# Optimization experiments

Measured on AMD Instinct MI355X. Metric: run time of the kernel, lower is better.

## Reference

```python
import jax, jax.numpy as jnp
import numpy as np

BATCH = 2048
NUM_FIELDS = 32
EMBED = 64
NPAIRS = NUM_FIELDS * (NUM_FIELDS - 1) // 2  # 496
# static pair indices (i < j), same order as the torch double loop
ROW, COL = np.triu_indices(NUM_FIELDS, k=1)
ROW = jnp.asarray(ROW)
COL = jnp.asarray(COL)


def setup_inputs() -> dict:
    key = jax.random.key(0)
    k1, k2 = jax.random.split(key)
    emb_inputs = jax.random.normal(k1, (BATCH, NUM_FIELDS, EMBED), dtype=jnp.float32)
    # xavier_normal_ on kernel of shape (E, NC2, E): fan_in = NC2*E (dims[1:]), fan_out = E*E... 
    # torch: fan_in = size(1)*receptive = NPAIRS*EMBED? torch uses size(1)*prod(size[2:]) = NPAIRS*EMBED,
    # fan_out = size(0)*prod(size[2:]) = EMBED*EMBED; std = sqrt(2/(fan_in+fan_out))
    fan_in = NPAIRS * EMBED
    fan_out = EMBED * EMBED
    std = float(np.sqrt(2.0 / (fan_in + fan_out)))
    kernel = jax.random.normal(k2, (EMBED, NPAIRS, EMBED), dtype=jnp.float32) * std
    return {"emb_inputs": emb_inputs, "kernel": kernel}


def reference(emb_inputs, kernel):
    # emb_inputs: (B, N, E); kernel: (E, NC2, E)
    p = emb_inputs[:, ROW]  # (B, NC2, E)
    q = emb_inputs[:, COL]  # (B, NC2, E)
    # torch: kp[b,i,pair] = sum_j p[b,pair,j] * kernel[i,pair,j]; out[b,pair] = sum_i kp*q
    kp = jnp.einsum('bpj,ipj->bpi', p, kernel)  # (B, NC2, E) -- avoids (B,E,NC2,E) blowup
    outputs = jnp.sum(kp * q, axis=-1)          # (B, NC2)
    return outputs[:, None, :]                  # (B, 1, NC2)
```

## Files before the change

### kernel.cpp

```cpp
#include <hip/hip_runtime.h>
#include <hip/hip_bf16.h>

#define BATCH   2048
#define NFIELDS 32
#define EMBED   64
#define NPAIRS  496

typedef __attribute__((ext_vector_type(8))) short bf16x8;
typedef __attribute__((ext_vector_type(4))) float f32x4;

__device__ __forceinline__ unsigned short f2bf(float x) {
    unsigned int u = __float_as_uint(x);
    unsigned int r = 0x7fffu + ((u >> 16) & 1u);
    return (unsigned short)((u + r) >> 16);
}
__device__ __forceinline__ bf16x8 cvt8(const float* p) {
    float4 v0 = *(const float4*)p;
    float4 v1 = *(const float4*)(p + 4);
    bf16x8 o;
    o[0]=(short)f2bf(v0.x); o[1]=(short)f2bf(v0.y); o[2]=(short)f2bf(v0.z); o[3]=(short)f2bf(v0.w);
    o[4]=(short)f2bf(v1.x); o[5]=(short)f2bf(v1.y); o[6]=(short)f2bf(v1.z); o[7]=(short)f2bf(v1.w);
    return o;
}

__global__ __launch_bounds__(256) void convert_prepass(
    const float* __restrict__ emb, const float* __restrict__ kern,
    unsigned short* __restrict__ embB, unsigned short* __restrict__ kernB)
{
    const int EMB4 = BATCH * NFIELDS * EMBED / 4;
    const int KER4 = EMBED * NPAIRS * EMBED / 4;
    int t = blockIdx.x * blockDim.x + threadIdx.x;
    if (t < EMB4) {
        float4 v = ((const float4*)emb)[t];
        ushort4 o;
        o.x = f2bf(v.x); o.y = f2bf(v.y); o.z = f2bf(v.z); o.w = f2bf(v.w);
        *(ushort4*)(embB + (size_t)t * 4) = o;
    } else if (t < EMB4 + KER4) {
        int u = t - EMB4;
        int j4   = u & 15;
        int rest = u >> 4;
        int p = rest % NPAIRS;
        int i = rest / NPAIRS;
        float4 v = *(const float4*)(kern + (size_t)i * (NPAIRS*EMBED) + (size_t)p * EMBED + j4*4);
        ushort4 o;
        o.x = f2bf(v.x); o.y = f2bf(v.y); o.z = f2bf(v.z); o.w = f2bf(v.w);
        *(ushort4*)(kernB + (size_t)p * 4096 + i * 64 + j4 * 4) = o;
    }
}

template<bool PRE>
__global__ __launch_bounds__(256) void opn_main(
    const void* __restrict__ embP, const void* __restrict__ kernP,
    const float* __restrict__ embF, float* __restrict__ out)
{
    const int chunk = blockIdx.x;
    const int bt    = blockIdx.y;
    const int tid   = threadIdx.x;
    const int wave  = tid >> 6, lane = tid & 63;
    const int col   = lane & 15, quad = lane >> 4;
    const int pair  = chunk * 4 + wave;

    int r = 0, s = 0;
    while (pair >= s + (NFIELDS - 1 - r)) { s += NFIELDS - 1 - r; ++r; }
    const int c = r + 1 + (pair - s);

    __shared__ __align__(16) float Otile[128][4];

    bf16x8 kfr[4][2];
    if (PRE) {
        const unsigned short* kb = (const unsigned short*)kernP + (size_t)pair * 4096;
        #pragma unroll
        for (int nt = 0; nt < 4; ++nt)
            #pragma unroll
            for (int ks = 0; ks < 2; ++ks)
                kfr[nt][ks] = *(const bf16x8*)(kb + (nt*16 + col) * 64 + ks*32 + quad*8);
    } else {
        const float* kf = (const float*)kernP;
        #pragma unroll
        for (int nt = 0; nt < 4; ++nt)
            #pragma unroll
            for (int ks = 0; ks < 2; ++ks)
                kfr[nt][ks] = cvt8(kf + (size_t)(nt*16 + col) * (NPAIRS*EMBED)
                                     + (size_t)pair * EMBED + ks*32 + quad*8);
    }

    #pragma unroll 2
    for (int it = 0; it < 8; ++it) {
        const int brow = bt * 128 + it * 16 + col;

        bf16x8 bfr0, bfr1;
        if (PRE) {
            const unsigned short* eb = (const unsigned short*)embP
                                     + ((size_t)brow * NFIELDS + r) * EMBED;
            bfr0 = *(const bf16x8*)(eb + quad*8);
            bfr1 = *(const bf16x8*)(eb + 32 + quad*8);
        } else {
            const float* ef = (const float*)embP + ((size_t)brow * NFIELDS + r) * EMBED;
            bfr0 = cvt8(ef + quad*8);
            bfr1 = cvt8(ef + 32 + quad*8);
        }

        const float* qp = embF + ((size_t)brow * NFIELDS + c) * EMBED + quad*4;
        f32x4 q0 = *(const f32x4*)(qp);
        f32x4 q1 = *(const f32x4*)(qp + 16);
        f32x4 q2 = *(const f32x4*)(qp + 32);
        f32x4 q3 = *(const f32x4*)(qp + 48);

        float partial = 0.f;
        #pragma unroll
        for (int nt = 0; nt < 4; ++nt) {
            f32x4 acc = {0.f, 0.f, 0.f, 0.f};
            acc = __builtin_amdgcn_mfma_f32_16x16x32_bf16(kfr[nt][0], bfr0, acc, 0, 0, 0);
            acc = __builtin_amdgcn_mfma_f32_16x16x32_bf16(kfr[nt][1], bfr1, acc, 0, 0, 0);
            f32x4 qq = (nt == 0) ? q0 : (nt == 1) ? q1 : (nt == 2) ? q2 : q3;
            partial += acc[0]*qq[0] + acc[1]*qq[1] + acc[2]*qq[2] + acc[3]*qq[3];
        }
        partial += __shfl_xor(partial, 16, 64);
        partial += __shfl_xor(partial, 32, 64);
        if (quad == 0) Otile[it*16 + col][wave] = partial;
    }
    __syncthreads();

    if (tid < 128) {
        f32x4 o = *(const f32x4*)&Otile[tid][0];
        *(f32x4*)&out[((size_t)(bt*128 + tid)) * NPAIRS + chunk*4] = o;
    }
}

extern "C" void kernel_launch(void* const* d_in, const int* in_sizes, int n_in,
                              void* d_out, int out_size, void* d_ws, size_t ws_size,
                              hipStream_t stream) {
    const float* emb  = (const float*)d_in[0];
    const float* kern = (const float*)d_in[1];
    float* out = (float*)d_out;

    const size_t embElems  = (size_t)BATCH * NFIELDS * EMBED;
    const size_t kernElems = (size_t)EMBED * NPAIRS * EMBED;
    const size_t need = (embElems + kernElems) * sizeof(unsigned short);

    dim3 grid(NPAIRS / 4, BATCH / 128);
    if (ws_size >= need) {
        unsigned short* embB  = (unsigned short*)d_ws;
        unsigned short* kernB = embB + embElems;
        int total4 = (int)((embElems + kernElems) / 4);
        convert_prepass<<<(total4 + 255) / 256, 256, 0, stream>>>(emb, kern, embB, kernB);
        opn_main<true><<<grid, 256, 0, stream>>>((const void*)embB, (const void*)kernB, emb, out);
    } else {
        opn_main<false><<<grid, 256, 0, stream>>>((const void*)emb, (const void*)kern, emb, out);
    }
}
```

Before: 125.8 us.

## Fuse bf16 conversion into main kernel, halve batch tile, swizzle block order

Drops the separate fp32-to-bf16 conversion prepass and workspace, so the main kernel reads fp32 embeddings and kernel weights directly and converts them in registers. The batch tile per block shrinks from 128 to 64 rows, doubling the grid to 3968 one-dimensional blocks, with a swizzled block index to group blocks for cache locality. This removes a launch and a full read/write pass over both tensors. In exchange, fp32 data is re-read at twice the width, and each block now reloads and converts its kernel fragments while amortising them over fewer rows.

```diff
diff --git a/kernel.cpp b/kernel.cpp
--- a/kernel.cpp
+++ b/kernel.cpp
@@ -23,84 +23,43 @@
     return o;
 }
 
-__global__ __launch_bounds__(256) void convert_prepass(
+__global__ __launch_bounds__(256) void opn_fused(
     const float* __restrict__ emb, const float* __restrict__ kern,
-    unsigned short* __restrict__ embB, unsigned short* __restrict__ kernB)
+    float* __restrict__ out)
 {
-    const int EMB4 = BATCH * NFIELDS * EMBED / 4;
-    const int KER4 = EMBED * NPAIRS * EMBED / 4;
-    int t = blockIdx.x * blockDim.x + threadIdx.x;
-    if (t < EMB4) {
-        float4 v = ((const float4*)emb)[t];
-        ushort4 o;
-        o.x = f2bf(v.x); o.y = f2bf(v.y); o.z = f2bf(v.z); o.w = f2bf(v.w);
-        *(ushort4*)(embB + (size_t)t * 4) = o;
-    } else if (t < EMB4 + KER4) {
-        int u = t - EMB4;
-        int j4   = u & 15;
-        int rest = u >> 4;
-        int p = rest % NPAIRS;
-        int i = rest / NPAIRS;
-        float4 v = *(const float4*)(kern + (size_t)i * (NPAIRS*EMBED) + (size_t)p * EMBED + j4*4);
-        ushort4 o;
-        o.x = f2bf(v.x); o.y = f2bf(v.y); o.z = f2bf(v.z); o.w = f2bf(v.w);
-        *(ushort4*)(kernB + (size_t)p * 4096 + i * 64 + j4 * 4) = o;
-    }
-}
+    const int bid = blockIdx.x;
+    const int swz = (bid & 7) * 496 + (bid >> 3);
+    const int chunk = swz >> 5;
+    const int bt    = swz & 31;
 
-template<bool PRE>
-__global__ __launch_bounds__(256) void opn_main(
-    const void* __restrict__ embP, const void* __restrict__ kernP,
-    const float* __restrict__ embF, float* __restrict__ out)
-{
-    const int chunk = blockIdx.x;
-    const int bt    = blockIdx.y;
-    const int tid   = threadIdx.x;
-    const int wave  = tid >> 6, lane = tid & 63;
-    const int col   = lane & 15, quad = lane >> 4;
-    const int pair  = chunk * 4 + wave;
+    const int tid  = threadIdx.x;
+    const int wave = tid >> 6, lane = tid & 63;
+    const int col  = lane & 15, quad = lane >> 4;
+    const int pair = chunk * 4 + wave;
 
     int r = 0, s = 0;
     while (pair >= s + (NFIELDS - 1 - r)) { s += NFIELDS - 1 - r; ++r; }
     const int c = r + 1 + (pair - s);
 
-    __shared__ __align__(16) float Otile[128][4];
+    __shared__ __align__(16) float Otile[64][4];
 
     bf16x8 kfr[4][2];
-    if (PRE) {
-        const unsigned short* kb = (const unsigned short*)kernP + (size_t)pair * 4096;
+    #pragma unroll
+    for (int nt = 0; nt < 4; ++nt)
         #pragma unroll
-        for (int nt = 0; nt < 4; ++nt)
-            #pragma unroll
-            for (int ks = 0; ks < 2; ++ks)
-                kfr[nt][ks] = *(const bf16x8*)(kb + (nt*16 + col) * 64 + ks*32 + quad*8);
-    } else {
-        const float* kf = (const float*)kernP;
-        #pragma unroll
-        for (int nt = 0; nt < 4; ++nt)
-            #pragma unroll
-            for (int ks = 0; ks < 2; ++ks)
-                kfr[nt][ks] = cvt8(kf + (size_t)(nt*16 + col) * (NPAIRS*EMBED)
-                                     + (size_t)pair * EMBED + ks*32 + quad*8);
-    }
+        for (int ks = 0; ks < 2; ++ks)
+            kfr[nt][ks] = cvt8(kern + (size_t)(nt*16 + col) * (NPAIRS*EMBED)
+                                 + (size_t)pair * EMBED + ks*32 + quad*8);
 
-    #pragma unroll 2
-    for (int it = 0; it < 8; ++it) {
-        const int brow = bt * 128 + it * 16 + col;
+    #pragma unroll
+    for (int it = 0; it < 4; ++it) {
+        const int brow = bt * 64 + it * 16 + col;
 
-        bf16x8 bfr0, bfr1;
-        if (PRE) {
-            const unsigned short* eb = (const unsigned short*)embP
-                                     + ((size_t)brow * NFIELDS + r) * EMBED;
-            bfr0 = *(const bf16x8*)(eb + quad*8);
-            bfr1 = *(const bf16x8*)(eb + 32 + quad*8);
-        } else {
-            const float* ef = (const float*)embP + ((size_t)brow * NFIELDS + r) * EMBED;
-            bfr0 = cvt8(ef + quad*8);
-            bfr1 = cvt8(ef + 32 + quad*8);
-        }
+        const float* ef = emb + ((size_t)brow * NFIELDS + r) * EMBED;
+        bf16x8 bfr0 = cvt8(ef + quad*8);
+        bf16x8 bfr1 = cvt8(ef + 32 + quad*8);
 
-        const float* qp = embF + ((size_t)brow * NFIELDS + c) * EMBED + quad*4;
+        const float* qp = emb + ((size_t)brow * NFIELDS + c) * EMBED + quad*4;
         f32x4 q0 = *(const f32x4*)(qp);
         f32x4 q1 = *(const f32x4*)(qp + 16);
         f32x4 q2 = *(const f32x4*)(qp + 32);
@@ -121,9 +80,9 @@
     }
     __syncthreads();
 
-    if (tid < 128) {
+    if (tid < 64) {
         f32x4 o = *(const f32x4*)&Otile[tid][0];
-        *(f32x4*)&out[((size_t)(bt*128 + tid)) * NPAIRS + chunk*4] = o;
+        *(f32x4*)&out[((size_t)(bt*64 + tid)) * NPAIRS + chunk*4] = o;
     }
 }
 
@@ -134,18 +93,5 @@
     const float* kern = (const float*)d_in[1];
     float* out = (float*)d_out;
 
-    const size_t embElems  = (size_t)BATCH * NFIELDS * EMBED;
-    const size_t kernElems = (size_t)EMBED * NPAIRS * EMBED;
-    const size_t need = (embElems + kernElems) * sizeof(unsigned short);
-
-    dim3 grid(NPAIRS / 4, BATCH / 128);
-    if (ws_size >= need) {
-        unsigned short* embB  = (unsigned short*)d_ws;
-        unsigned short* kernB = embB + embElems;
-        int total4 = (int)((embElems + kernElems) / 4);
-        convert_prepass<<<(total4 + 255) / 256, 256, 0, stream>>>(emb, kern, embB, kernB);
-        opn_main<true><<<grid, 256, 0, stream>>>((const void*)embB, (const void*)kernB, emb, out);
-    } else {
-        opn_main<false><<<grid, 256, 0, stream>>>((const void*)emb, (const void*)kern, emb, out);
-    }
+    opn_fused<<<dim3(3968), 256, 0, stream>>>(emb, kern, out);
 }
```

After: 151.6 us. 20.5% more time.

## Halve batch tile, swizzle block order for XCD locality, read q from bf16

Applied to the files above, without the earlier changes.

Each block now covers 64 batch rows instead of 128, on a flattened 3968-block grid. Block IDs are remapped so consecutive blocks on the same XCD (bid mod 8) take contiguous chunk/batch tiles, which should improve L2 reuse of kernel and embedding data. The q operand now comes from the bf16 converted embedding copy instead of the fp32 original, cutting its memory traffic in half at the cost of bf16 rounding on q. The smaller tile doubles the number of kernel-fragment loads per pair in exchange for more blocks and better occupancy balance.

```diff
diff --git a/kernel.cpp b/kernel.cpp
--- a/kernel.cpp
+++ b/kernel.cpp
@@ -13,6 +13,9 @@
     unsigned int u = __float_as_uint(x);
     unsigned int r = 0x7fffu + ((u >> 16) & 1u);
     return (unsigned short)((u + r) >> 16);
+}
+__device__ __forceinline__ float bf2f(unsigned short b) {
+    return __uint_as_float(((unsigned int)b) << 16);
 }
 __device__ __forceinline__ bf16x8 cvt8(const float* p) {
     float4 v0 = *(const float4*)p;
@@ -49,22 +52,25 @@
 }
 
 template<bool PRE>
-__global__ __launch_bounds__(256) void opn_main(
+__global__ __launch_bounds__(256) void opn_fused(
     const void* __restrict__ embP, const void* __restrict__ kernP,
     const float* __restrict__ embF, float* __restrict__ out)
 {
-    const int chunk = blockIdx.x;
-    const int bt    = blockIdx.y;
-    const int tid   = threadIdx.x;
-    const int wave  = tid >> 6, lane = tid & 63;
-    const int col   = lane & 15, quad = lane >> 4;
-    const int pair  = chunk * 4 + wave;
+    const int bid = blockIdx.x;
+    const int swz = (bid & 7) * 496 + (bid >> 3);
+    const int chunk = swz >> 5;
+    const int bt    = swz & 31;
+
+    const int tid  = threadIdx.x;
+    const int wave = tid >> 6, lane = tid & 63;
+    const int col  = lane & 15, quad = lane >> 4;
+    const int pair = chunk * 4 + wave;
 
     int r = 0, s = 0;
     while (pair >= s + (NFIELDS - 1 - r)) { s += NFIELDS - 1 - r; ++r; }
     const int c = r + 1 + (pair - s);
 
-    __shared__ __align__(16) float Otile[128][4];
+    __shared__ __align__(16) float Otile[64][4];
 
     bf16x8 kfr[4][2];
     if (PRE) {
@@ -84,27 +90,36 @@
                                      + (size_t)pair * EMBED + ks*32 + quad*8);
     }
 
-    #pragma unroll 2
-    for (int it = 0; it < 8; ++it) {
-        const int brow = bt * 128 + it * 16 + col;
+    #pragma unroll
+    for (int it = 0; it < 4; ++it) {
+        const int brow = bt * 64 + it * 16 + col;
 
         bf16x8 bfr0, bfr1;
+        float qf[4][4];
         if (PRE) {
             const unsigned short* eb = (const unsigned short*)embP
                                      + ((size_t)brow * NFIELDS + r) * EMBED;
             bfr0 = *(const bf16x8*)(eb + quad*8);
             bfr1 = *(const bf16x8*)(eb + 32 + quad*8);
+            const unsigned short* qb = (const unsigned short*)embP
+                                     + ((size_t)brow * NFIELDS + c) * EMBED + quad*4;
+            #pragma unroll
+            for (int nt = 0; nt < 4; ++nt) {
+                ushort4 qv = *(const ushort4*)(qb + nt*16);
+                qf[nt][0] = bf2f(qv.x); qf[nt][1] = bf2f(qv.y);
+                qf[nt][2] = bf2f(qv.z); qf[nt][3] = bf2f(qv.w);
+            }
         } else {
             const float* ef = (const float*)embP + ((size_t)brow * NFIELDS + r) * EMBED;
             bfr0 = cvt8(ef + quad*8);
             bfr1 = cvt8(ef + 32 + quad*8);
+            const float* qp = embF + ((size_t)brow * NFIELDS + c) * EMBED + quad*4;
+            #pragma unroll
+            for (int nt = 0; nt < 4; ++nt) {
+                f32x4 qv = *(const f32x4*)(qp + nt*16);
+                qf[nt][0] = qv[0]; qf[nt][1] = qv[1]; qf[nt][2] = qv[2]; qf[nt][3] = qv[3];
+            }
         }
-
-        const float* qp = embF + ((size_t)brow * NFIELDS + c) * EMBED + quad*4;
-        f32x4 q0 = *(const f32x4*)(qp);
-        f32x4 q1 = *(const f32x4*)(qp + 16);
-        f32x4 q2 = *(const f32x4*)(qp + 32);
-        f32x4 q3 = *(const f32x4*)(qp + 48);
 
         float partial = 0.f;
         #pragma unroll
@@ -112,8 +127,7 @@
             f32x4 acc = {0.f, 0.f, 0.f, 0.f};
             acc = __builtin_amdgcn_mfma_f32_16x16x32_bf16(kfr[nt][0], bfr0, acc, 0, 0, 0);
             acc = __builtin_amdgcn_mfma_f32_16x16x32_bf16(kfr[nt][1], bfr1, acc, 0, 0, 0);
-            f32x4 qq = (nt == 0) ? q0 : (nt == 1) ? q1 : (nt == 2) ? q2 : q3;
-            partial += acc[0]*qq[0] + acc[1]*qq[1] + acc[2]*qq[2] + acc[3]*qq[3];
+            partial += acc[0]*qf[nt][0] + acc[1]*qf[nt][1] + acc[2]*qf[nt][2] + acc[3]*qf[nt][3];
         }
         partial += __shfl_xor(partial, 16, 64);
         partial += __shfl_xor(partial, 32, 64);
@@ -121,9 +135,9 @@
     }
     __syncthreads();
 
-    if (tid < 128) {
+    if (tid < 64) {
         f32x4 o = *(const f32x4*)&Otile[tid][0];
-        *(f32x4*)&out[((size_t)(bt*128 + tid)) * NPAIRS + chunk*4] = o;
+        *(f32x4*)&out[((size_t)(bt*64 + tid)) * NPAIRS + chunk*4] = o;
     }
 }
 
@@ -138,14 +152,15 @@
     const size_t kernElems = (size_t)EMBED * NPAIRS * EMBED;
     const size_t need = (embElems + kernElems) * sizeof(unsigned short);
 
-    dim3 grid(NPAIRS / 4, BATCH / 128);
     if (ws_size >= need) {
         unsigned short* embB  = (unsigned short*)d_ws;
         unsigned short* kernB = embB + embElems;
         int total4 = (int)((embElems + kernElems) / 4);
         convert_prepass<<<(total4 + 255) / 256, 256, 0, stream>>>(emb, kern, embB, kernB);
-        opn_main<true><<<grid, 256, 0, stream>>>((const void*)embB, (const void*)kernB, emb, out);
+        opn_fused<true><<<dim3(3968), 256, 0, stream>>>(
+            (const void*)embB, (const void*)kernB, emb, out);
     } else {
-        opn_main<false><<<grid, 256, 0, stream>>>((const void*)emb, (const void*)kern, emb, out);
+        opn_fused<false><<<dim3(3968), 256, 0, stream>>>(
+            (const void*)emb, (const void*)kern, emb, out);
     }
 }
```

New measurement: 129.7 us. 3.1% more time.
